# Kernel tuning notes

Hardware: AMD Instinct MI355X
Metric: run time of the kernel (lower is better)

The kernel has to match this reference:

```python
import jax, jax.numpy as jnp
import numpy as np

B, N, C, H = 4, 1024, 1024, 16
HD = C // H
SCALE = HD ** -0.5


def _init_linear(key, out_dim, in_dim):
    # torch nn.Linear default init: U(-1/sqrt(in), 1/sqrt(in)) for weight and bias
    kw, kb = jax.random.split(key)
    bound = 1.0 / np.sqrt(in_dim)
    W = jax.random.uniform(kw, (out_dim, in_dim), jnp.float32, -bound, bound)
    b = jax.random.uniform(kb, (out_dim,), jnp.float32, -bound, bound)
    return W, b


def setup_inputs() -> dict:
    key = jax.random.key(0)
    ks = jax.random.split(key, 5)
    x = jax.random.normal(ks[0], (B, N, C), jnp.float32)
    # NdLinear qkv: Linear(N->N) along seq axis, then Linear(C->3C) along channel axis
    Wq0, bq0 = _init_linear(ks[1], N, N)
    Wq1, bq1 = _init_linear(ks[2], 3 * C, C)
    # NdLinear proj: Linear(N->N) along seq axis, then Linear(C->C) along channel axis
    Wp0, bp0 = _init_linear(ks[3], N, N)
    Wp1, bp1 = _init_linear(ks[4], C, C)
    return {"x": x, "Wq0": Wq0, "bq0": bq0, "Wq1": Wq1, "bq1": bq1,
            "Wp0": Wp0, "bp0": bp0, "Wp1": Wp1, "bp1": bp1}


def _ndlinear(x, W0, b0, W1, b1):
    # NdLinear over (seq, channel): apply Linear along axis 1, then axis 2.
    # torch Linear: y = x @ W.T + b
    x = jnp.einsum('bnc,mn->bmc', x, W0) + b0[None, :, None]   # seq axis
    x = jnp.einsum('bnc,dc->bnd', x, W1) + b1                  # channel axis
    return x


def reference(x, Wq0, bq0, Wq1, bq1, Wp0, bp0, Wp1, bp1):
    qkv = _ndlinear(x, Wq0, bq0, Wq1, bq1)                     # (B, N, 3C)
    qkv = qkv.reshape(B, N, 3, H, HD).transpose(2, 0, 3, 1, 4) # (3, B, H, N, HD)
    q, k, v = qkv[0], qkv[1], qkv[2]
    attn = jnp.einsum('bhnd,bhmd->bhnm', q, k) * SCALE         # (B, H, N, N)
    attn = jax.nn.softmax(attn, axis=-1)
    out = jnp.einsum('bhnm,bhmd->bhnd', attn, v)               # (B, H, N, HD)
    out = out.transpose(0, 2, 1, 3).reshape(B, N, C)
    out = _ndlinear(out, Wp0, bp0, Wp1, bp1)
    return out
```

## Files before the change

kernel.cpp:

```cpp
#include <hip/hip_runtime.h>
#include <hip/hip_bf16.h>
#include <stdint.h>

typedef __bf16 bf16;
typedef __bf16 bf16x4 __attribute__((ext_vector_type(4)));
typedef __bf16 bf16x8 __attribute__((ext_vector_type(8)));
typedef float f32x4 __attribute__((ext_vector_type(4)));

#define B_ 4
#define N_ 1024
#define C_ 1024
#define H_ 16
#define MEG (1u << 20)

__device__ __forceinline__ uint32_t lds_off(const void* p) {
    return (uint32_t)(uintptr_t)p;
}
__device__ __forceinline__ void g2l16(const void* g, uint32_t lds_byte) {
    __builtin_amdgcn_global_load_lds(
        (const __attribute__((address_space(1))) unsigned int*)(uintptr_t)g,
        (__attribute__((address_space(3))) unsigned int*)(uintptr_t)lds_byte,
        16, 0, 0);
}

__global__ __launch_bounds__(256) void prep_k(
    const float* __restrict__ x, bf16* __restrict__ xT,
    const float* __restrict__ s0, bf16* __restrict__ d0,
    const float* __restrict__ s1, bf16* __restrict__ d1,
    const float* __restrict__ s2, bf16* __restrict__ d2,
    const float* __restrict__ s3, bf16* __restrict__ d3)
{
    __shared__ bf16 t[64][66];
    const int bid = blockIdx.x;
    const int tid = threadIdx.x;
    if (bid < 3072) {
        const float* s; bf16* d; int base;
        if (bid < 512)       { s = s0; d = d0; base = 0; }
        else if (bid < 2048) { s = s1; d = d1; base = 512; }
        else if (bid < 2560) { s = s2; d = d2; base = 2048; }
        else                 { s = s3; d = d3; base = 2560; }
        int i = ((bid - base) * 256 + tid) * 8;
        float4 a = *(const float4*)(s + i);
        float4 b = *(const float4*)(s + i + 4);
        bf16x8 r;
        r[0] = (bf16)a.x; r[1] = (bf16)a.y; r[2] = (bf16)a.z; r[3] = (bf16)a.w;
        r[4] = (bf16)b.x; r[5] = (bf16)b.y; r[6] = (bf16)b.z; r[7] = (bf16)b.w;
        *(bf16x8*)(d + i) = r;
        return;
    }
    const int idx = bid - 3072;
    const int c0 = (idx & 15) * 64, n0 = ((idx >> 4) & 15) * 64, b = idx >> 8;
    {
        int nl = tid >> 2, seg = tid & 3;
        const float* src = x + ((size_t)b * N_ + n0 + nl) * C_ + c0 + seg * 16;
#pragma unroll
        for (int i = 0; i < 4; ++i) {
            float4 v = *(const float4*)(src + i * 4);
            t[nl][seg * 16 + i * 4 + 0] = (bf16)v.x;
            t[nl][seg * 16 + i * 4 + 1] = (bf16)v.y;
            t[nl][seg * 16 + i * 4 + 2] = (bf16)v.z;
            t[nl][seg * 16 + i * 4 + 3] = (bf16)v.w;
        }
    }
    __syncthreads();
    {
        int cl = tid >> 2, seg = tid & 3;
        bf16* dst = xT + ((size_t)b * C_ + c0 + cl) * N_ + n0 + seg * 16;
        bf16x8 o0, o1;
#pragma unroll
        for (int j = 0; j < 8; ++j) o0[j] = t[seg * 16 + j][cl];
#pragma unroll
        for (int j = 0; j < 8; ++j) o1[j] = t[seg * 16 + 8 + j][cl];
        *(bf16x8*)dst = o0;
        *(bf16x8*)(dst + 8) = o1;
    }
}

template <int BIAS, bool OF32>
__global__ __launch_bounds__(512) void gemm_k(
    const bf16* __restrict__ A, const bf16* __restrict__ Bm,
    const float* __restrict__ bias, void* __restrict__ Cv,
    int M, int Nn, int K, long long sA, long long sB, long long sC)
{
    __shared__ bf16 smem[2][2][128 * 64];

    const int tid = threadIdx.x;
    const int lane = tid & 63, wid = tid >> 6;
    const int lr = lane & 15, lg = lane >> 4;
    const int wr = wid >> 2, wc = wid & 3;
    const int m0 = blockIdx.y * 128, n0 = blockIdx.x * 128;

    const bf16* Ab = A + (size_t)blockIdx.z * sA;
    const bf16* Bb = Bm + (size_t)blockIdx.z * sB;

    const uint32_t a_lds0 = lds_off(&smem[0][0][0]);
    const uint32_t b_lds0 = lds_off(&smem[0][1][0]);
    const uint32_t bufstride = 2 * 128 * 64 * 2;

    auto stage = [&](int kt, int buf) {
#pragma unroll
        for (int half = 0; half < 2; ++half) {
            int it = tid + half * 512;
            int r = it >> 3, ch = it & 7;
            int sch = ch ^ (r & 7);
            g2l16(Ab + (size_t)(m0 + r) * K + kt * 64 + sch * 8,
                  a_lds0 + buf * bufstride + it * 16);
            g2l16(Bb + (size_t)(n0 + r) * K + kt * 64 + sch * 8,
                  b_lds0 + buf * bufstride + it * 16);
        }
    };

    f32x4 acc[4][2];
#pragma unroll
    for (int i = 0; i < 4; ++i)
#pragma unroll
        for (int j = 0; j < 2; ++j) { f32x4 z = {0.f,0.f,0.f,0.f}; acc[i][j] = z; }

    stage(0, 0);
    __syncthreads();

    const int nt = K >> 6;
    for (int t = 0; t < nt; ++t) {
        int buf = t & 1;
        if (t + 1 < nt) stage(t + 1, buf ^ 1);
        const bf16* As = &smem[buf][0][0];
        const bf16* Bs = &smem[buf][1][0];
#pragma unroll
        for (int s = 0; s < 2; ++s) {
            bf16x8 af[4], bfr[2];
#pragma unroll
            for (int mi = 0; mi < 4; ++mi) {
                int row = wr * 64 + mi * 16 + lr;
                int slot = (s * 4 + lg) ^ (row & 7);
                af[mi] = *(const bf16x8*)(As + row * 64 + slot * 8);
            }
#pragma unroll
            for (int ni = 0; ni < 2; ++ni) {
                int row = wc * 32 + ni * 16 + lr;
                int slot = (s * 4 + lg) ^ (row & 7);
                bfr[ni] = *(const bf16x8*)(Bs + row * 64 + slot * 8);
            }
#pragma unroll
            for (int mi = 0; mi < 4; ++mi)
#pragma unroll
                for (int ni = 0; ni < 2; ++ni)
                    acc[mi][ni] = __builtin_amdgcn_mfma_f32_16x16x32_bf16(
                        af[mi], bfr[ni], acc[mi][ni], 0, 0, 0);
        }
        __syncthreads();
    }

#pragma unroll
    for (int mi = 0; mi < 4; ++mi)
#pragma unroll
        for (int ni = 0; ni < 2; ++ni)
#pragma unroll
            for (int r = 0; r < 4; ++r) {
                int row = m0 + wr * 64 + mi * 16 + lg * 4 + r;
                int col = n0 + wc * 32 + ni * 16 + lr;
                float bv = (BIAS == 0) ? bias[row] : bias[col];
                float v = acc[mi][ni][r] + bv;
                if constexpr (OF32)
                    ((float*)Cv + (size_t)blockIdx.z * sC)[(size_t)row * Nn + col] = v;
                else
                    ((bf16*)Cv + (size_t)blockIdx.z * sC)[(size_t)row * Nn + col] = (bf16)v;
            }
}

__global__ __launch_bounds__(256) void attn_k(
    const bf16* __restrict__ qkv, bf16* __restrict__ aoT)
{
    __shared__ bf16 Ks[2][4096];
    __shared__ bf16 Vs[2][4096];
    __shared__ bf16 pbuf[4][1024];

    const int tid = threadIdx.x;
    const int lane = tid & 63, wid = tid >> 6;
    const int lr = lane & 15, lg = lane >> 4;
    const int bid = blockIdx.x;
    const int qt = bid >> 6, hb = bid & 63;
    const int b = hb >> 4, h = hb & 15;
    const int qrow0 = qt * 64 + wid * 16;
    const int hoff = h * 64;
    const bf16* qkvb = qkv + (size_t)b * (N_ * 3 * C_);

    bf16x8 qf[2];
#pragma unroll
    for (int kk = 0; kk < 2; ++kk) {
        qf[kk] = *(const bf16x8*)(qkvb + (size_t)(qrow0 + lr) * 3072 +
                                  hoff + kk * 32 + lg * 8);
#pragma unroll
        for (int j = 0; j < 8; ++j)
            qf[kk][j] = (bf16)((float)qf[kk][j] * 0.18033688f);
    }

    const uint32_t ks0 = lds_off(&Ks[0][0]);
    const int vd = tid & 63, vkg = tid >> 6;

    auto stageK = [&](int kt, int buf) {
#pragma unroll
        for (int hh = 0; hh < 2; ++hh) {
            int it = tid + hh * 256;
            int key = it >> 3, ch = it & 7;
            int sch = ch ^ (key & 7);
            g2l16(qkvb + (size_t)(kt * 64 + key) * 3072 + C_ + hoff + sch * 8,
                  ks0 + buf * 8192 + it * 16);
        }
    };
    auto loadV = [&](int kt, bf16x8 v[2]) {
        const bf16* base = qkvb + 2 * C_ + hoff + vd;
#pragma unroll
        for (int hh = 0; hh < 2; ++hh) {
            int kg = vkg + hh * 4;
#pragma unroll
            for (int j = 0; j < 8; ++j)
                v[hh][j] = base[(size_t)(kt * 64 + kg * 8 + j) * 3072];
        }
    };
    auto writeV = [&](bf16x8 v[2], int buf) {
#pragma unroll
        for (int hh = 0; hh < 2; ++hh) {
            int kg = vkg + hh * 4;
            *(bf16x8*)(&Vs[buf][vd * 64 + ((kg ^ (vd & 7)) * 8)]) = v[hh];
        }
    };

    float lsum = 0.f;
    f32x4 o[4];
#pragma unroll
    for (int i = 0; i < 4; ++i) { f32x4 z = {0.f,0.f,0.f,0.f}; o[i] = z; }

    char* prow = (char*)&pbuf[wid][0] + lr * 128;
    const int swz = (lr & 7) << 4;

    bf16x8 v0buf[2];
    stageK(0, 0);
    loadV(0, v0buf);
    writeV(v0buf, 0);
    __syncthreads();

    for (int kt = 0; kt < 16; ++kt) {
        int buf = kt & 1;
        bf16x8 vnext[2];
        if (kt + 1 < 16) {
            stageK(kt + 1, buf ^ 1);
            loadV(kt + 1, vnext);
        }

        f32x4 s[4];
        __builtin_amdgcn_s_setprio(1);
#pragma unroll
        for (int st = 0; st < 4; ++st) {
            f32x4 z = {0.f, 0.f, 0.f, 0.f};
#pragma unroll
            for (int kk = 0; kk < 2; ++kk) {
                int row = st * 16 + lr;
                int slot = (kk * 4 + lg) ^ (row & 7);
                bf16x8 kf = *(const bf16x8*)(&Ks[buf][row * 64 + slot * 8]);
                z = __builtin_amdgcn_mfma_f32_16x16x32_bf16(kf, qf[kk], z, 0, 0, 0);
            }
            s[st] = z;
        }
        __builtin_amdgcn_s_setprio(0);

#pragma unroll
        for (int st = 0; st < 4; ++st) {
            bf16x4 w;
#pragma unroll
            for (int r = 0; r < 4; ++r) {
                float e = __builtin_amdgcn_exp2f(s[st][r]);
                w[r] = (bf16)e;
                lsum += e;
            }
            *(bf16x4*)(prow + ((st * 32 + lg * 8) ^ swz)) = w;
        }

        bf16x8 pf[2];
        pf[0] = *(const bf16x8*)(prow + ((lg * 16) ^ swz));
        pf[1] = *(const bf16x8*)(prow + ((64 + lg * 16) ^ swz));

        __builtin_amdgcn_s_setprio(1);
#pragma unroll
        for (int dt = 0; dt < 4; ++dt) {
            int row = dt * 16 + lr;
            bf16x8 v0 = *(const bf16x8*)(&Vs[buf][row * 64 + ((lg ^ (lr & 7)) * 8)]);
            bf16x8 v1 = *(const bf16x8*)(&Vs[buf][row * 64 + (((4 + lg) ^ (lr & 7)) * 8)]);
            o[dt] = __builtin_amdgcn_mfma_f32_16x16x32_bf16(pf[0], v0, o[dt], 0, 0, 0);
            o[dt] = __builtin_amdgcn_mfma_f32_16x16x32_bf16(pf[1], v1, o[dt], 0, 0, 0);
        }
        __builtin_amdgcn_s_setprio(0);

        if (kt + 1 < 16) writeV(vnext, buf ^ 1);
        __syncthreads();
    }

    lsum += __shfl_xor(lsum, 16, 64);
    lsum += __shfl_xor(lsum, 32, 64);
    float rtot = 1.0f / lsum;
    float rcpo[4];
#pragma unroll
    for (int r = 0; r < 4; ++r) rcpo[r] = __shfl(rtot, lg * 4 + r, 64);

#pragma unroll
    for (int dt = 0; dt < 4; ++dt) {
        bf16x4 ov;
#pragma unroll
        for (int r = 0; r < 4; ++r) ov[r] = (bf16)(o[dt][r] * rcpo[r]);
        size_t c = (size_t)b * C_ + hoff + dt * 16 + lr;
        *(bf16x4*)(aoT + c * N_ + qrow0 + lg * 4) = ov;
    }
}

extern "C" void kernel_launch(void* const* d_in, const int* in_sizes, int n_in,
                              void* d_out, int out_size, void* d_ws, size_t ws_size,
                              hipStream_t stream) {
    (void)in_sizes; (void)n_in; (void)out_size; (void)ws_size;
    const float* x   = (const float*)d_in[0];
    const float* Wq0 = (const float*)d_in[1];
    const float* bq0 = (const float*)d_in[2];
    const float* Wq1 = (const float*)d_in[3];
    const float* bq1 = (const float*)d_in[4];
    const float* Wp0 = (const float*)d_in[5];
    const float* bp0 = (const float*)d_in[6];
    const float* Wp1 = (const float*)d_in[7];
    const float* bp1 = (const float*)d_in[8];

    bf16* ws   = (bf16*)d_ws;
    bf16* xT   = ws;
    bf16* Wq0b = ws + 4 * MEG;
    bf16* Wq1b = ws + 5 * MEG;
    bf16* Wp0b = ws + 8 * MEG;
    bf16* Wp1b = ws + 9 * MEG;
    bf16* y1   = ws + 10 * MEG;
    bf16* y2   = ws + 14 * MEG;
    bf16* aoT  = y1;
    bf16* z1   = y2;
    float* outp = (float*)d_out;

    const long long s1M = (long long)N_ * C_;

    prep_k<<<dim3(4096), 256, 0, stream>>>(x, xT, Wq0, Wq0b, Wq1, Wq1b,
                                           Wp0, Wp0b, Wp1, Wp1b);

    gemm_k<0, false><<<dim3(8, 8, 4), 512, 0, stream>>>(
        Wq0b, xT, bq0, y1, 1024, 1024, 1024, 0LL, s1M, s1M);
    gemm_k<1, false><<<dim3(24, 32, 1), 512, 0, stream>>>(
        y1, Wq1b, bq1, y2, 4096, 3072, 1024, 0LL, 0LL, 0LL);
    attn_k<<<dim3(1024), 256, 0, stream>>>(y2, aoT);
    gemm_k<0, false><<<dim3(8, 8, 4), 512, 0, stream>>>(
        Wp0b, aoT, bp0, z1, 1024, 1024, 1024, 0LL, s1M, s1M);
    gemm_k<1, true><<<dim3(8, 32, 1), 512, 0, stream>>>(
        z1, Wp1b, bp1, outp, 4096, 1024, 1024, 0LL, 0LL, 0LL);
}
```

Baseline: 123.1 us.

## Write V transposed from QKV GEMM epilogue and async-stage it in attention

The channel-projection GEMM epilogue now writes the V part of QKV in a transposed per-batch layout (d-major, sequence contiguous) into a reused workspace buffer. The attention kernel then loads V tiles with async global-to-LDS 16-byte copies, matching the K path, instead of strided scalar gathers through registers followed by LDS writes. The aim is to remove uncoalesced V loads and register pressure in attention. In exchange, the GEMM epilogue does scattered 8-byte transposed stores for the V columns.

After: 119.9 us. 1.03x faster.

```diff
diff --git a/kernel.cpp b/kernel.cpp
--- a/kernel.cpp
+++ b/kernel.cpp
@@ -76,10 +76,11 @@
     }
 }
 
-template <int BIAS, bool OF32>
+template <int BIAS, bool OF32, bool VSPLIT>
 __global__ __launch_bounds__(512) void gemm_k(
     const bf16* __restrict__ A, const bf16* __restrict__ Bm,
     const float* __restrict__ bias, void* __restrict__ Cv,
+    bf16* __restrict__ vT,
     int M, int Nn, int K, long long sA, long long sB, long long sC)
 {
     __shared__ bf16 smem[2][2][128 * 64];
@@ -153,11 +154,24 @@
 #pragma unroll
     for (int mi = 0; mi < 4; ++mi)
 #pragma unroll
-        for (int ni = 0; ni < 2; ++ni)
+        for (int ni = 0; ni < 2; ++ni) {
+            int col = n0 + wc * 32 + ni * 16 + lr;
+            if constexpr (VSPLIT) {
+                if (col >= 2048) {
+                    float bv = bias[col];
+                    bf16x4 w;
+#pragma unroll
+                    for (int r = 0; r < 4; ++r) w[r] = (bf16)(acc[mi][ni][r] + bv);
+                    int row0 = m0 + wr * 64 + mi * 16 + lg * 4;
+                    int bb = row0 >> 10, n = row0 & 1023;
+                    *(bf16x4*)(vT + (size_t)bb * MEG +
+                               (size_t)(col - 2048) * 1024 + n) = w;
+                    continue;
+                }
+            }
 #pragma unroll
             for (int r = 0; r < 4; ++r) {
                 int row = m0 + wr * 64 + mi * 16 + lg * 4 + r;
-                int col = n0 + wc * 32 + ni * 16 + lr;
                 float bv = (BIAS == 0) ? bias[row] : bias[col];
                 float v = acc[mi][ni][r] + bv;
                 if constexpr (OF32)
@@ -165,10 +179,12 @@
                 else
                     ((bf16*)Cv + (size_t)blockIdx.z * sC)[(size_t)row * Nn + col] = (bf16)v;
             }
+        }
 }
 
 __global__ __launch_bounds__(256) void attn_k(
-    const bf16* __restrict__ qkv, bf16* __restrict__ aoT)
+    const bf16* __restrict__ qkv, const bf16* __restrict__ vT,
+    bf16* __restrict__ aoT)
 {
     __shared__ bf16 Ks[2][4096];
     __shared__ bf16 Vs[2][4096];
@@ -183,6 +199,7 @@
     const int qrow0 = qt * 64 + wid * 16;
     const int hoff = h * 64;
     const bf16* qkvb = qkv + (size_t)b * (N_ * 3 * C_);
+    const bf16* vTb  = vT + (size_t)b * MEG;
 
     bf16x8 qf[2];
 #pragma unroll
@@ -195,7 +212,7 @@
     }
 
     const uint32_t ks0 = lds_off(&Ks[0][0]);
-    const int vd = tid & 63, vkg = tid >> 6;
+    const uint32_t vs0 = lds_off(&Vs[0][0]);
 
     auto stageK = [&](int kt, int buf) {
 #pragma unroll
@@ -207,21 +224,14 @@
                   ks0 + buf * 8192 + it * 16);
         }
     };
-    auto loadV = [&](int kt, bf16x8 v[2]) {
-        const bf16* base = qkvb + 2 * C_ + hoff + vd;
+    auto stageV = [&](int kt, int buf) {
 #pragma unroll
         for (int hh = 0; hh < 2; ++hh) {
-            int kg = vkg + hh * 4;
-#pragma unroll
-            for (int j = 0; j < 8; ++j)
-                v[hh][j] = base[(size_t)(kt * 64 + kg * 8 + j) * 3072];
-        }
-    };
-    auto writeV = [&](bf16x8 v[2], int buf) {
-#pragma unroll
-        for (int hh = 0; hh < 2; ++hh) {
-            int kg = vkg + hh * 4;
-            *(bf16x8*)(&Vs[buf][vd * 64 + ((kg ^ (vd & 7)) * 8)]) = v[hh];
+            int it = tid + hh * 256;
+            int d = it >> 3, ch = it & 7;
+            int sch = ch ^ (d & 7);
+            g2l16(vTb + (size_t)(hoff + d) * 1024 + kt * 64 + sch * 8,
+                  vs0 + buf * 8192 + it * 16);
         }
     };
 
@@ -233,18 +243,15 @@
     char* prow = (char*)&pbuf[wid][0] + lr * 128;
     const int swz = (lr & 7) << 4;
 
-    bf16x8 v0buf[2];
     stageK(0, 0);
-    loadV(0, v0buf);
-    writeV(v0buf, 0);
+    stageV(0, 0);
     __syncthreads();
 
     for (int kt = 0; kt < 16; ++kt) {
         int buf = kt & 1;
-        bf16x8 vnext[2];
         if (kt + 1 < 16) {
             stageK(kt + 1, buf ^ 1);
-            loadV(kt + 1, vnext);
+            stageV(kt + 1, buf ^ 1);
         }
 
         f32x4 s[4];
@@ -290,7 +297,6 @@
         }
         __builtin_amdgcn_s_setprio(0);
 
-        if (kt + 1 < 16) writeV(vnext, buf ^ 1);
         __syncthreads();
     }
 
@@ -333,6 +339,7 @@
     bf16* Wp1b = ws + 9 * MEG;
     bf16* y1   = ws + 10 * MEG;
     bf16* y2   = ws + 14 * MEG;
+    bf16* vT   = xT;
     bf16* aoT  = y1;
     bf16* z1   = y2;
     float* outp = (float*)d_out;
@@ -342,13 +349,13 @@
     prep_k<<<dim3(4096), 256, 0, stream>>>(x, xT, Wq0, Wq0b, Wq1, Wq1b,
                                            Wp0, Wp0b, Wp1, Wp1b);
 
-    gemm_k<0, false><<<dim3(8, 8, 4), 512, 0, stream>>>(
-        Wq0b, xT, bq0, y1, 1024, 1024, 1024, 0LL, s1M, s1M);
-    gemm_k<1, false><<<dim3(24, 32, 1), 512, 0, stream>>>(
-        y1, Wq1b, bq1, y2, 4096, 3072, 1024, 0LL, 0LL, 0LL);
-    attn_k<<<dim3(1024), 256, 0, stream>>>(y2, aoT);
-    gemm_k<0, false><<<dim3(8, 8, 4), 512, 0, stream>>>(
-        Wp0b, aoT, bp0, z1, 1024, 1024, 1024, 0LL, s1M, s1M);
-    gemm_k<1, true><<<dim3(8, 32, 1), 512, 0, stream>>>(
-        z1, Wp1b, bp1, outp, 4096, 1024, 1024, 0LL, 0LL, 0LL);
-}
+    gemm_k<0, false, false><<<dim3(8, 8, 4), 512, 0, stream>>>(
+        Wq0b, xT, bq0, y1, nullptr, 1024, 1024, 1024, 0LL, s1M, s1M);
+    gemm_k<1, false, true><<<dim3(24, 32, 1), 512, 0, stream>>>(
+        y1, Wq1b, bq1, y2, vT, 4096, 3072, 1024, 0LL, 0LL, 0LL);
+    attn_k<<<dim3(1024), 256, 0, stream>>>(y2, vT, aoT);
+    gemm_k<0, false, false><<<dim3(8, 8, 4), 512, 0, stream>>>(
+        Wp0b, aoT, bp0, z1, nullptr, 1024, 1024, 1024, 0LL, s1M, s1M);
+    gemm_k<1, true, false><<<dim3(8, 32, 1), 512, 0, stream>>>(
+        z1, Wp1b, bp1, outp, nullptr, 4096, 1024, 1024, 0LL, 0LL, 0LL);
+}
```
